# Performance work log

Hardware: AMD Instinct MI355X
Metric: run time of the kernel (lower is better)

## Reference

```python
import jax, jax.numpy as jnp
import numpy as np

CHUNK = 64
EMA_DECAY = 0.99


def setup_inputs() -> dict:
    key = jax.random.key(0)
    ks = jax.random.split(key, 4)
    Bsz, S, H, P, N = 2, 4096, 16, 64, 128
    X = jax.random.normal(ks[0], (Bsz, S, H, P), jnp.float32)
    # negative log-decay rates, as in Mamba-2 (A = -softplus(...) style)
    A = -jnp.abs(jax.random.normal(ks[1], (Bsz, S, H), jnp.float32)) * 0.1
    Bm = jax.random.normal(ks[2], (Bsz, S, H, N), jnp.float32) / np.sqrt(N)
    Cm = jax.random.normal(ks[3], (Bsz, S, H, N), jnp.float32) / np.sqrt(N)
    # ChunkedSurpriseGate parameters / buffers
    log2_alpha_base = jnp.full((H,), -0.15, jnp.float32)
    log2_beta = jnp.zeros((H,), jnp.float32)
    surprise_ema = jnp.ones((H,), jnp.float32)
    return {"X": X, "A": A, "Bm": Bm, "Cm": Cm,
            "log2_alpha_base": log2_alpha_base, "log2_beta": log2_beta,
            "surprise_ema": surprise_ema}


def _chunked_surprise_ssd(X, A, Bm, Cm, log2_alpha_base, log2_beta, surprise_ema):
    Bsz, S, H, P = X.shape
    N = Bm.shape[-1]
    cs = CHUNK
    nC = S // cs  # seqlen chosen divisible by chunk_size (no padding branch)

    # [B, nC, cs, H, ...] -> chunk-major [nC, B, H, cs, ...] for lax.scan
    Xc = X.reshape(Bsz, nC, cs, H, P).transpose(1, 0, 3, 2, 4)   # [nC,B,H,cs,P]
    Ac = A.reshape(Bsz, nC, cs, H).transpose(1, 0, 3, 2)          # [nC,B,H,cs]
    Bc = Bm.reshape(Bsz, nC, cs, H, N).transpose(1, 0, 3, 2, 4)   # [nC,B,H,cs,N]
    Cc = Cm.reshape(Bsz, nC, cs, H, N).transpose(1, 0, 3, 2, 4)   # [nC,B,H,cs,N]

    idx = jnp.arange(cs)
    tri = idx[:, None] >= idx[None, :]  # causal mask for decay matrix L

    # gate constants (per-head)
    alpha_base = 1.0 - jnp.exp2(jnp.clip(log2_alpha_base, -3.32, -0.015))  # [H]
    beta = jnp.exp2(jnp.clip(log2_beta, -2.0, 2.0))                         # [H]

    def step(carry, xs):
        h_prev, h_before, decay_prev, ema = carry
        c, X_c, A_c, B_c, C_c = xs
        first = c == 0

        # --- delayed state-based surprise: ||h_prev - decay_prev * h_before||^2
        err = jnp.mean((h_prev - decay_prev[..., None, None] * h_before) ** 2,
                       axis=(-2, -1))  # [B,H]
        # EMA update (training=True path; torch does it under no_grad)
        ema_new = jax.lax.stop_gradient(EMA_DECAY * ema + (1.0 - EMA_DECAY) * jnp.mean(err, axis=0))
        normalized = err / (ema_new[None, :] + 1e-6)                # [B,H]
        boost = jax.nn.relu(jnp.tanh(beta[None, :] * normalized))
        alpha = jnp.clip(alpha_base[None, :] + (1.0 - alpha_base[None, :]) * boost,
                         0.01, 0.999)
        # torch: decay_scale = (1-alpha).mean().item()  -> detached scalar
        ds = jax.lax.stop_gradient(jnp.mean(1.0 - alpha))
        decay_scale = jnp.where(first, jnp.float32(1.0), ds)
        ema_out = jnp.where(first, ema, ema_new)  # no gate call on chunk 0

        # --- single-chunk SSD ---
        Acs = jnp.cumsum(A_c * decay_scale, axis=-1)                 # [B,H,cs]
        # causal decay matrix L[i,j] = exp(Acs[i]-Acs[j]) for i>=j
        L = jnp.where(tri, jnp.exp(Acs[..., :, None] - Acs[..., None, :]), 0.0)
        CB = jnp.einsum('bhin,bhjn->bhij', C_c, B_c)
        Y_intra = jnp.einsum('bhij,bhjd->bhid', L * CB, X_c)
        decay_from_start = jnp.exp(Acs)                               # [B,H,cs]
        Y_inter = jnp.einsum('bhin,bhnd,bhi->bhid', C_c, h_prev, decay_from_start)
        decay_to_end = jnp.exp(Acs[..., -1:] - Acs)                   # [B,H,cs]
        h_contrib = jnp.einsum('bhtn,bhtd,bht->bhnd', B_c, X_c, decay_to_end)
        decay_total = jnp.exp(Acs[..., -1])                           # [B,H]
        h_end = decay_total[..., None, None] * h_prev + h_contrib

        return (h_end, h_prev, decay_total, ema_out), Y_intra + Y_inter

    h0 = jnp.zeros((Bsz, H, N, P), X.dtype)
    carry0 = (h0, h0, jnp.ones((Bsz, H), X.dtype), surprise_ema)
    xs = (jnp.arange(nC), Xc, Ac, Bc, Cc)
    _, Ys = jax.lax.scan(step, carry0, xs)  # [nC,B,H,cs,P]

    # stack dim=2, permute(0,2,3,1,4), reshape -> [B,S,H,P]
    Y = Ys.transpose(1, 0, 3, 2, 4).reshape(Bsz, S, H, P)
    return Y


def reference(X, A, Bm, Cm, log2_alpha_base, log2_beta, surprise_ema):
    return _chunked_surprise_ssd(X, A, Bm, Cm, log2_alpha_base, log2_beta, surprise_ema)
```

## Files before the change

### kernel.cpp

```cpp
#include <hip/hip_runtime.h>
#include <math.h>


#define CSZ 64
#define NCH 64
#define NHD 16
#define PD  64
#define ND  128
#define BHN 32
#define NTILES 2048
#define GGRID 64
#define SEQ 4096

#define WS_S   0
#define WS_EG  131072
#define WS_DS  262144
#define WS_HC  262400

using bf16x8 = __attribute__((ext_vector_type(8))) short;
using f32x4  = __attribute__((ext_vector_type(4))) float;

__device__ __forceinline__ short f2bf(float f) {
  union { float f; unsigned u; } v; v.f = f;
  unsigned r = (v.u + 0x7FFFu + ((v.u >> 16) & 1u)) >> 16;
  return (short)r;
}

__device__ __forceinline__ float bf2f(short s) {
  union { float f; unsigned u; } v;
  v.u = ((unsigned)(unsigned short)s) << 16;
  return v.f;
}

__device__ __forceinline__ void split4(float4 v, short4& hi, short4& lo) {
  hi.x = f2bf(v.x); lo.x = f2bf(v.x - bf2f(hi.x));
  hi.y = f2bf(v.y); lo.y = f2bf(v.y - bf2f(hi.y));
  hi.z = f2bf(v.z); lo.z = f2bf(v.z - bf2f(hi.z));
  hi.w = f2bf(v.w); lo.w = f2bf(v.w - bf2f(hi.w));
}

__global__ __launch_bounds__(256) void k_gramerr(
    const float* __restrict__ X, const float* __restrict__ A,
    const float* __restrict__ Bm, float* __restrict__ ws)
{
  __shared__ __align__(16) short BhiS[64*136];
  __shared__ __align__(16) short BloS[64*136];
  __shared__ __align__(16) short XhiS[64*72];
  __shared__ __align__(16) short XloS[64*72];
  __shared__ float Sl[CSZ];
  __shared__ float Zl[CSZ];
  short* Mhi = BhiS;
  short* Mlo = BloS;
  short* Uhi = XhiS;
  short* Ulo = XloS;

  const int tile = blockIdx.x;
  const int c  = tile & 63;
  const int bh = tile >> 6;
  const int b = bh >> 4, h = bh & 15;
  const int tid = threadIdx.x;

  if (tid < CSZ) {
    float v = A[(size_t)(b*SEQ + c*CSZ + tid)*NHD + h];
    #pragma unroll
    for (int d = 1; d < 64; d <<= 1) {
      float n = __shfl_up(v, d);
      if (tid >= d) v += n;
    }
    Sl[tid] = v;
    ws[WS_S + tile*CSZ + tid] = v;
  }

  {
    const float* Bbase = Bm + ((size_t)(b*SEQ + c*CSZ)*NHD + h)*ND;
    #pragma unroll
    for (int qq = 0; qq < 8; ++qq) {
      int lin = qq*256 + tid;
      int t = lin >> 5, n4 = (lin & 31)*4;
      float4 v = *(const float4*)(Bbase + (size_t)t*(NHD*ND) + n4);
      short4 hi, lo; split4(v, hi, lo);
      *(short4*)&BhiS[t*136 + n4] = hi;
      *(short4*)&BloS[t*136 + n4] = lo;
    }
    const float* Xbase = X + ((size_t)(b*SEQ + c*CSZ)*NHD + h)*PD;
    #pragma unroll
    for (int qq = 0; qq < 4; ++qq) {
      int lin = qq*256 + tid;
      int t = lin >> 4, p4 = (lin & 15)*4;
      float4 v = *(const float4*)(Xbase + (size_t)t*(NHD*PD) + p4);
      short4 hi, lo; split4(v, hi, lo);
      *(short4*)&XhiS[t*72 + p4] = hi;
      *(short4*)&XloS[t*72 + p4] = lo;
    }
  }
  __syncthreads();

  if (tid < CSZ) Zl[tid] = Sl[63] - Sl[tid];

  const int w = tid >> 6;
  const int lane = tid & 63;
  const int m = lane & 15, q = lane >> 4;

  f32x4 z4 = {0.f,0.f,0.f,0.f};
  f32x4 gb[4], gx[4];
  #pragma unroll
  for (int i = 0; i < 4; ++i) { gb[i] = z4; gx[i] = z4; }

  #pragma unroll
  for (int kk = 0; kk < 4; ++kk) {
    const int ao = (w*16+m)*136 + kk*32 + q*8;
    bf16x8 ah = *(bf16x8*)&BhiS[ao];
    bf16x8 al = *(bf16x8*)&BloS[ao];
    #pragma unroll
    for (int ct = 0; ct < 4; ++ct) {
      const int bo = (ct*16+m)*136 + kk*32 + q*8;
      bf16x8 bhv = *(bf16x8*)&BhiS[bo];
      bf16x8 blv = *(bf16x8*)&BloS[bo];
      gb[ct] = __builtin_amdgcn_mfma_f32_16x16x32_bf16(ah, bhv, gb[ct], 0,0,0);
      gb[ct] = __builtin_amdgcn_mfma_f32_16x16x32_bf16(ah, blv, gb[ct], 0,0,0);
      gb[ct] = __builtin_amdgcn_mfma_f32_16x16x32_bf16(al, bhv, gb[ct], 0,0,0);
    }
  }
  #pragma unroll
  for (int kk = 0; kk < 2; ++kk) {
    const int ao = (w*16+m)*72 + kk*32 + q*8;
    bf16x8 ah = *(bf16x8*)&XhiS[ao];
    bf16x8 al = *(bf16x8*)&XloS[ao];
    #pragma unroll
    for (int ct = 0; ct < 4; ++ct) {
      const int bo = (ct*16+m)*72 + kk*32 + q*8;
      bf16x8 bhv = *(bf16x8*)&XhiS[bo];
      bf16x8 blv = *(bf16x8*)&XloS[bo];
      gx[ct] = __builtin_amdgcn_mfma_f32_16x16x32_bf16(ah, bhv, gx[ct], 0,0,0);
      gx[ct] = __builtin_amdgcn_mfma_f32_16x16x32_bf16(ah, blv, gx[ct], 0,0,0);
      gx[ct] = __builtin_amdgcn_mfma_f32_16x16x32_bf16(al, bhv, gx[ct], 0,0,0);
    }
  }
  __syncthreads();

  #pragma unroll
  for (int ct = 0; ct < 4; ++ct)
    #pragma unroll
    for (int r = 0; r < 4; ++r) {
      int i = w*16 + q*4 + r;
      int j = ct*16 + m;
      float mvf = gb[ct][r]*gx[ct][r]*(1.0f/8192.0f);
      short mh = f2bf(mvf);
      Mhi[i*72 + j] = mh;
      Mlo[i*72 + j] = f2bf(mvf - bf2f(mh));
    }
  #pragma unroll
  for (int qq = 0; qq < 16; ++qq) {
    int idx = qq*256 + tid;
    int g = idx >> 6, t = idx & 63;
    float u = expf(((float)g*(1.0f/63.0f))*Zl[t]);
    short uh = f2bf(u);
    Uhi[g*72 + t] = uh;
    Ulo[g*72 + t] = f2bf(u - bf2f(uh));
  }
  __syncthreads();

  f32x4 wv4[4];
  #pragma unroll
  for (int i = 0; i < 4; ++i) wv4[i] = z4;
  #pragma unroll
  for (int kk = 0; kk < 2; ++kk) {
    const int ao = (w*16+m)*72 + kk*32 + q*8;
    bf16x8 uh = *(bf16x8*)&Uhi[ao];
    bf16x8 ul = *(bf16x8*)&Ulo[ao];
    #pragma unroll
    for (int ct = 0; ct < 4; ++ct) {
      const int bo = (ct*16+m)*72 + kk*32 + q*8;
      bf16x8 mh = *(bf16x8*)&Mhi[bo];
      bf16x8 ml = *(bf16x8*)&Mlo[bo];
      wv4[ct] = __builtin_amdgcn_mfma_f32_16x16x32_bf16(uh, mh, wv4[ct], 0,0,0);
      wv4[ct] = __builtin_amdgcn_mfma_f32_16x16x32_bf16(uh, ml, wv4[ct], 0,0,0);
      wv4[ct] = __builtin_amdgcn_mfma_f32_16x16x32_bf16(ul, mh, wv4[ct], 0,0,0);
    }
  }

  #pragma unroll
  for (int r = 0; r < 4; ++r) {
    int g = w*16 + q*4 + r;
    float e = 0.f;
    #pragma unroll
    for (int ct = 0; ct < 4; ++ct) {
      int t = ct*16 + m;
      float uval = bf2f(Uhi[g*72 + t]) + bf2f(Ulo[g*72 + t]);
      e += wv4[ct][r] * uval;
    }
    e += __shfl_xor(e, 1);
    e += __shfl_xor(e, 2);
    e += __shfl_xor(e, 4);
    e += __shfl_xor(e, 8);
    if (m == 0) ws[WS_EG + (c*GGRID + g)*BHN + bh] = e;
  }
}

__global__ __launch_bounds__(64) void k_gate(
    const float* __restrict__ l2ab, const float* __restrict__ l2b,
    const float* __restrict__ sema, float* __restrict__ ws)
{
  const int lane = threadIdx.x;
  const int h = lane & 15;
  float ab = 0.f, bt = 1.f, ema = 0.f;
  if (lane < NHD) {
    float la = fminf(fmaxf(l2ab[lane], -3.32f), -0.015f);
    ab = 1.0f - exp2f(la);
    float lb = fminf(fmaxf(l2b[lane], -2.0f), 2.0f);
    bt = exp2f(lb);
    ema = sema[lane];
  }
  const float ab_bh = __shfl(ab, h);
  const float bt_bh = __shfl(bt, h);
  float ds_prev = 1.0f;
  if (lane == 0) ws[WS_DS + 0] = 1.0f;
  const float* EG = ws + WS_EG;
  for (int c = 1; c < NCH; ++c) {
    const int j = c - 1;
    float x = ds_prev * 63.0f;
    int ib = (int)floorf(x);
    ib = max(1, min(61, ib));
    float u = x - (float)ib;
    float err = 0.f;
    if (lane < BHN) {
      const float* p = EG + ((size_t)j*GGRID + (ib-1))*BHN + lane;
      float ym1 = p[0], y0 = p[32], y1 = p[64], y2 = p[96];
      err = ym1*(u*(u-1.f)*(u-2.f))*(-1.f/6.f)
          + y0 *((u+1.f)*(u-1.f)*(u-2.f))*(0.5f)
          + y1 *((u+1.f)*u*(u-2.f))*(-0.5f)
          + y2 *((u+1.f)*u*(u-1.f))*(1.f/6.f);
    }
    float e0 = __shfl(err, h);
    float e1 = __shfl(err, 16 + h);
    float ema_new = 0.99f*ema + 0.01f*0.5f*(e0 + e1);
    float emv = __shfl(ema_new, h);
    float oma = 0.f;
    if (lane < BHN) {
      float normalized = err / (emv + 1e-6f);
      float boost = fmaxf(tanhf(bt_bh*normalized), 0.f);
      float alpha = ab_bh + (1.f - ab_bh)*boost;
      alpha = fminf(fmaxf(alpha, 0.01f), 0.999f);
      oma = 1.f - alpha;
    }
    float s = oma;
    s += __shfl_xor(s, 1);  s += __shfl_xor(s, 2);  s += __shfl_xor(s, 4);
    s += __shfl_xor(s, 8);  s += __shfl_xor(s, 16);
    float ds = __shfl(s, 0) * (1.0f/32.0f);
    if (lane < NHD) ema = ema_new;
    if (lane == 0) ws[WS_DS + c] = ds;
    ds_prev = ds;
  }
}

__global__ __launch_bounds__(256, 2) void k_chunk(
    const float* __restrict__ X, const float* __restrict__ Bm,
    const float* __restrict__ Cm, float* __restrict__ ws,
    float* __restrict__ Y)
{
  __shared__ short Cs[64*136];
  __shared__ short Bs[64*136];
  __shared__ short BsTw[128*72];
  __shared__ short XsT[64*72];
  __shared__ short Es[64*72];
  __shared__ float Acs[CSZ];
  __shared__ float Wl[CSZ];

  const int tile = blockIdx.x;
  const int c  = tile & 63;
  const int bh = tile >> 6;
  const int b = bh >> 4, h = bh & 15;
  const int tid = threadIdx.x;

  const float dsc = ws[WS_DS + c];
  if (tid < CSZ) {
    float sv  = ws[WS_S + tile*CSZ + tid];
    float s63 = ws[WS_S + tile*CSZ + 63];
    Acs[tid] = dsc*sv;
    Wl[tid]  = expf(dsc*(s63 - sv));
  }
  __syncthreads();

  const float* Bbase = Bm + ((size_t)(b*SEQ + c*CSZ)*NHD + h)*ND;
  const float* Cbase = Cm + ((size_t)(b*SEQ + c*CSZ)*NHD + h)*ND;
  const float* Xbase = X  + ((size_t)(b*SEQ + c*CSZ)*NHD + h)*PD;
  #pragma unroll
  for (int qq = 0; qq < 8; ++qq) {
    int lin = qq*256 + tid;
    int t = lin >> 5, n4 = (lin & 31)*4;
    float4 cv = *(const float4*)(Cbase + (size_t)t*(NHD*ND) + n4);
    short4 cs4; cs4.x=f2bf(cv.x); cs4.y=f2bf(cv.y); cs4.z=f2bf(cv.z); cs4.w=f2bf(cv.w);
    *(short4*)&Cs[t*136 + n4] = cs4;
    float4 bv = *(const float4*)(Bbase + (size_t)t*(NHD*ND) + n4);
    short4 bs4; bs4.x=f2bf(bv.x); bs4.y=f2bf(bv.y); bs4.z=f2bf(bv.z); bs4.w=f2bf(bv.w);
    *(short4*)&Bs[t*136 + n4] = bs4;
    float wt = Wl[t];
    BsTw[(n4+0)*72 + t] = f2bf(bv.x*wt);
    BsTw[(n4+1)*72 + t] = f2bf(bv.y*wt);
    BsTw[(n4+2)*72 + t] = f2bf(bv.z*wt);
    BsTw[(n4+3)*72 + t] = f2bf(bv.w*wt);
  }
  #pragma unroll
  for (int qq = 0; qq < 4; ++qq) {
    int lin = qq*256 + tid;
    int t = lin >> 4, p4 = (lin & 15)*4;
    float4 xv = *(const float4*)(Xbase + (size_t)t*(NHD*PD) + p4);
    XsT[(p4+0)*72 + t] = f2bf(xv.x);
    XsT[(p4+1)*72 + t] = f2bf(xv.y);
    XsT[(p4+2)*72 + t] = f2bf(xv.z);
    XsT[(p4+3)*72 + t] = f2bf(xv.w);
  }
  __syncthreads();

  const int w = tid >> 6;
  const int lane = tid & 63;
  const int m = lane & 15, q = lane >> 4;

  f32x4 acc0 = {0.f,0.f,0.f,0.f}, acc1 = acc0, acc2 = acc0, acc3 = acc0;
  #pragma unroll
  for (int kk = 0; kk < 4; ++kk) {
    bf16x8 af = *(bf16x8*)&Cs[(w*16+m)*136 + kk*32 + q*8];
    bf16x8 b0 = *(bf16x8*)&Bs[( 0+m)*136 + kk*32 + q*8];
    bf16x8 b1 = *(bf16x8*)&Bs[(16+m)*136 + kk*32 + q*8];
    bf16x8 b2 = *(bf16x8*)&Bs[(32+m)*136 + kk*32 + q*8];
    bf16x8 b3 = *(bf16x8*)&Bs[(48+m)*136 + kk*32 + q*8];
    acc0 = __builtin_amdgcn_mfma_f32_16x16x32_bf16(af, b0, acc0, 0,0,0);
    acc1 = __builtin_amdgcn_mfma_f32_16x16x32_bf16(af, b1, acc1, 0,0,0);
    acc2 = __builtin_amdgcn_mfma_f32_16x16x32_bf16(af, b2, acc2, 0,0,0);
    acc3 = __builtin_amdgcn_mfma_f32_16x16x32_bf16(af, b3, acc3, 0,0,0);
  }
  {
    f32x4 accs[4] = {acc0, acc1, acc2, acc3};
    #pragma unroll
    for (int ct = 0; ct < 4; ++ct) {
      int j = ct*16 + m;
      float aj = Acs[j];
      #pragma unroll
      for (int r = 0; r < 4; ++r) {
        int i = w*16 + q*4 + r;
        float v = (i >= j) ? expf(Acs[i]-aj)*accs[ct][r] : 0.f;
        Es[i*72 + j] = f2bf(v);
      }
    }
  }

  f32x4 h00={0.f,0.f,0.f,0.f}, h01=h00, h02=h00, h03=h00;
  f32x4 h10=h00, h11=h00, h12=h00, h13=h00;
  #pragma unroll
  for (int kk = 0; kk < 2; ++kk) {
    bf16x8 a0 = *(bf16x8*)&BsTw[((2*w+0)*16+m)*72 + kk*32 + q*8];
    bf16x8 a1 = *(bf16x8*)&BsTw[((2*w+1)*16+m)*72 + kk*32 + q*8];
    bf16x8 x0 = *(bf16x8*)&XsT[( 0+m)*72 + kk*32 + q*8];
    bf16x8 x1 = *(bf16x8*)&XsT[(16+m)*72 + kk*32 + q*8];
    bf16x8 x2 = *(bf16x8*)&XsT[(32+m)*72 + kk*32 + q*8];
    bf16x8 x3 = *(bf16x8*)&XsT[(48+m)*72 + kk*32 + q*8];
    h00 = __builtin_amdgcn_mfma_f32_16x16x32_bf16(a0, x0, h00, 0,0,0);
    h01 = __builtin_amdgcn_mfma_f32_16x16x32_bf16(a0, x1, h01, 0,0,0);
    h02 = __builtin_amdgcn_mfma_f32_16x16x32_bf16(a0, x2, h02, 0,0,0);
    h03 = __builtin_amdgcn_mfma_f32_16x16x32_bf16(a0, x3, h03, 0,0,0);
    h10 = __builtin_amdgcn_mfma_f32_16x16x32_bf16(a1, x0, h10, 0,0,0);
    h11 = __builtin_amdgcn_mfma_f32_16x16x32_bf16(a1, x1, h11, 0,0,0);
    h12 = __builtin_amdgcn_mfma_f32_16x16x32_bf16(a1, x2, h12, 0,0,0);
    h13 = __builtin_amdgcn_mfma_f32_16x16x32_bf16(a1, x3, h13, 0,0,0);
  }

  f32x4 y0={0.f,0.f,0.f,0.f}, y1=y0, y2=y0, y3=y0;
  #pragma unroll
  for (int kk = 0; kk < 2; ++kk) {
    bf16x8 ef = *(bf16x8*)&Es[(w*16+m)*72 + kk*32 + q*8];
    bf16x8 x0 = *(bf16x8*)&XsT[( 0+m)*72 + kk*32 + q*8];
    bf16x8 x1 = *(bf16x8*)&XsT[(16+m)*72 + kk*32 + q*8];
    bf16x8 x2 = *(bf16x8*)&XsT[(32+m)*72 + kk*32 + q*8];
    bf16x8 x3 = *(bf16x8*)&XsT[(48+m)*72 + kk*32 + q*8];
    y0 = __builtin_amdgcn_mfma_f32_16x16x32_bf16(ef, x0, y0, 0,0,0);
    y1 = __builtin_amdgcn_mfma_f32_16x16x32_bf16(ef, x1, y1, 0,0,0);
    y2 = __builtin_amdgcn_mfma_f32_16x16x32_bf16(ef, x2, y2, 0,0,0);
    y3 = __builtin_amdgcn_mfma_f32_16x16x32_bf16(ef, x3, y3, 0,0,0);
  }

  {
    float* Ybase = Y + ((size_t)(b*SEQ + c*CSZ)*NHD + h)*PD;
    f32x4 ys[4] = {y0, y1, y2, y3};
    #pragma unroll
    for (int r = 0; r < 4; ++r) {
      int i = w*16 + q*4 + r;
      #pragma unroll
      for (int ct = 0; ct < 4; ++ct)
        Ybase[(size_t)i*(NHD*PD) + ct*16 + m] = ys[ct][r];
    }
  }
  {
    float* hcp = ws + WS_HC + (size_t)tile*(ND*PD);
    f32x4 hs[2][4] = {{h00,h01,h02,h03},{h10,h11,h12,h13}};
    #pragma unroll
    for (int nt = 0; nt < 2; ++nt)
      #pragma unroll
      for (int r = 0; r < 4; ++r) {
        int n = (2*w+nt)*16 + q*4 + r;
        #pragma unroll
        for (int pt = 0; pt < 4; ++pt)
          hcp[n*PD + pt*16 + m] = hs[nt][pt][r];
      }
  }
}

__global__ __launch_bounds__(256) void k_scan(float* __restrict__ ws)
{
  __shared__ float dtbl[NCH];
  const int bh = blockIdx.x >> 3, part = blockIdx.x & 7;
  const int tid = threadIdx.x;
  if (tid < NCH) {
    float s63 = ws[WS_S + (bh*NCH + tid)*CSZ + 63];
    dtbl[tid] = expf(ws[WS_DS + tid]*s63);
  }
  __syncthreads();
  float* base = ws + WS_HC + (size_t)bh*(NCH*ND*PD) + part*1024 + tid*4;
  float4 h4 = make_float4(0.f, 0.f, 0.f, 0.f);
  #pragma unroll 1
  for (int c = 0; c < NCH; ++c) {
    float4* p = (float4*)(base + (size_t)c*(ND*PD));
    float4 v = *p;
    *p = h4;
    float dt = dtbl[c];
    h4.x = dt*h4.x + v.x;  h4.y = dt*h4.y + v.y;
    h4.z = dt*h4.z + v.z;  h4.w = dt*h4.w + v.w;
  }
}

__global__ __launch_bounds__(256, 4) void k_inter(
    const float* __restrict__ Cm, float* __restrict__ ws,
    float* __restrict__ Y)
{
  __shared__ short Cs[64*136];
  __shared__ short HsT[64*136];
  __shared__ float Dfs[CSZ];

  const int tile = blockIdx.x;
  const int c  = tile & 63;
  const int bh = tile >> 6;
  const int b = bh >> 4, h = bh & 15;
  const int tid = threadIdx.x;

  const float dsc = ws[WS_DS + c];
  if (tid < CSZ) Dfs[tid] = expf(dsc*ws[WS_S + tile*CSZ + tid]);

  const float* Cbase = Cm + ((size_t)(b*SEQ + c*CSZ)*NHD + h)*ND;
  const float* hp = ws + WS_HC + (size_t)tile*(ND*PD);
  #pragma unroll
  for (int qq = 0; qq < 8; ++qq) {
    int lin = qq*256 + tid;
    int t = lin >> 5, n4 = (lin & 31)*4;
    float4 cv = *(const float4*)(Cbase + (size_t)t*(NHD*ND) + n4);
    short4 cs4; cs4.x=f2bf(cv.x); cs4.y=f2bf(cv.y); cs4.z=f2bf(cv.z); cs4.w=f2bf(cv.w);
    *(short4*)&Cs[t*136 + n4] = cs4;
    int n = lin >> 4, p4 = (lin & 15)*4;
    float4 hv = *(const float4*)(hp + (size_t)lin*4);
    HsT[(p4+0)*136 + n] = f2bf(hv.x);
    HsT[(p4+1)*136 + n] = f2bf(hv.y);
    HsT[(p4+2)*136 + n] = f2bf(hv.z);
    HsT[(p4+3)*136 + n] = f2bf(hv.w);
  }
  __syncthreads();

  const int w = tid >> 6;
  const int lane = tid & 63;
  const int m = lane & 15, q = lane >> 4;

  f32x4 a0 = {0.f,0.f,0.f,0.f}, a1 = a0, a2 = a0, a3 = a0;
  #pragma unroll
  for (int kk = 0; kk < 4; ++kk) {
    bf16x8 cf = *(bf16x8*)&Cs[(w*16+m)*136 + kk*32 + q*8];
    bf16x8 hb0 = *(bf16x8*)&HsT[( 0+m)*136 + kk*32 + q*8];
    bf16x8 hb1 = *(bf16x8*)&HsT[(16+m)*136 + kk*32 + q*8];
    bf16x8 hb2 = *(bf16x8*)&HsT[(32+m)*136 + kk*32 + q*8];
    bf16x8 hb3 = *(bf16x8*)&HsT[(48+m)*136 + kk*32 + q*8];
    a0 = __builtin_amdgcn_mfma_f32_16x16x32_bf16(cf, hb0, a0, 0,0,0);
    a1 = __builtin_amdgcn_mfma_f32_16x16x32_bf16(cf, hb1, a1, 0,0,0);
    a2 = __builtin_amdgcn_mfma_f32_16x16x32_bf16(cf, hb2, a2, 0,0,0);
    a3 = __builtin_amdgcn_mfma_f32_16x16x32_bf16(cf, hb3, a3, 0,0,0);
  }

  float* Ybase = Y + ((size_t)(b*SEQ + c*CSZ)*NHD + h)*PD;
  f32x4 as[4] = {a0, a1, a2, a3};
  #pragma unroll
  for (int r = 0; r < 4; ++r) {
    int i = w*16 + q*4 + r;
    float d = Dfs[i];
    #pragma unroll
    for (int ct = 0; ct < 4; ++ct) {
      size_t idx = (size_t)i*(NHD*PD) + ct*16 + m;
      Ybase[idx] += d*as[ct][r];
    }
  }
}

extern "C" void kernel_launch(void* const* d_in, const int* in_sizes, int n_in,
                              void* d_out, int out_size, void* d_ws, size_t ws_size,
                              hipStream_t stream) {
  const float* X    = (const float*)d_in[0];
  const float* A    = (const float*)d_in[1];
  const float* Bm   = (const float*)d_in[2];
  const float* Cm   = (const float*)d_in[3];
  const float* l2ab = (const float*)d_in[4];
  const float* l2b  = (const float*)d_in[5];
  const float* sema = (const float*)d_in[6];
  float* Y  = (float*)d_out;
  float* ws = (float*)d_ws;

  hipLaunchKernelGGL(k_gramerr, dim3(NTILES), dim3(256), 0, stream, X, A, Bm, ws);
  hipLaunchKernelGGL(k_gate,    dim3(1),      dim3(64),  0, stream, l2ab, l2b, sema, ws);
  hipLaunchKernelGGL(k_chunk,   dim3(NTILES), dim3(256), 0, stream, X, Bm, Cm, ws, Y);
  hipLaunchKernelGGL(k_scan,    dim3(256),    dim3(256), 0, stream, ws);
  hipLaunchKernelGGL(k_inter,   dim3(NTILES), dim3(256), 0, stream, Cm, ws, Y);
}
```

Baseline: 344.8 us.

## Stage gate error grid in LDS, load C fragments directly, widen scan grid

In k_gate, the per-chunk error grid is double-buffered in shared memory with a register prefetch of the next chunk, so the serial loop no longer waits on dependent global loads. In k_chunk, the C operand is loaded straight from global memory into MFMA fragments in registers, and the Es buffer reuses the Bs buffer (with an added barrier). Dropping two LDS arrays lets launch bounds rise to 3 blocks per CU. k_scan runs on 4x more blocks with scalar instead of float4 elements, giving more parallelism to the latency-bound recurrence, at the cost of narrower memory accesses.

Result: slower. 367.4 us (+6.6%).

```diff
diff --git a/kernel.cpp b/kernel.cpp
--- a/kernel.cpp
+++ b/kernel.cpp
@@ -201,6 +201,7 @@
     const float* __restrict__ l2ab, const float* __restrict__ l2b,
     const float* __restrict__ sema, float* __restrict__ ws)
 {
+  __shared__ float EGs[2][GGRID*BHN];
   const int lane = threadIdx.x;
   const int h = lane & 15;
   float ab = 0.f, bt = 1.f, ema = 0.f;
@@ -213,18 +214,30 @@
   }
   const float ab_bh = __shfl(ab, h);
   const float bt_bh = __shfl(bt, h);
+  const float* EG = ws + WS_EG;
+  {
+    const float4* src = (const float4*)EG;
+    float4* dst = (float4*)EGs[0];
+    #pragma unroll
+    for (int r = 0; r < 8; ++r) dst[r*64 + lane] = src[r*64 + lane];
+  }
   float ds_prev = 1.0f;
   if (lane == 0) ws[WS_DS + 0] = 1.0f;
-  const float* EG = ws + WS_EG;
   for (int c = 1; c < NCH; ++c) {
-    const int j = c - 1;
+    const int cur = (c - 1) & 1;
+    float4 pf[8];
+    if (c < NCH-1) {
+      const float4* src = (const float4*)(EG + (size_t)c*(GGRID*BHN));
+      #pragma unroll
+      for (int r = 0; r < 8; ++r) pf[r] = src[r*64 + lane];
+    }
     float x = ds_prev * 63.0f;
     int ib = (int)floorf(x);
     ib = max(1, min(61, ib));
     float u = x - (float)ib;
     float err = 0.f;
     if (lane < BHN) {
-      const float* p = EG + ((size_t)j*GGRID + (ib-1))*BHN + lane;
+      const float* p = &EGs[cur][(ib-1)*BHN + lane];
       float ym1 = p[0], y0 = p[32], y1 = p[64], y2 = p[96];
       err = ym1*(u*(u-1.f)*(u-2.f))*(-1.f/6.f)
           + y0 *((u+1.f)*(u-1.f)*(u-2.f))*(0.5f)
@@ -250,27 +263,46 @@
     if (lane < NHD) ema = ema_new;
     if (lane == 0) ws[WS_DS + c] = ds;
     ds_prev = ds;
-  }
-}
-
-__global__ __launch_bounds__(256, 2) void k_chunk(
+    if (c < NCH-1) {
+      float4* dst = (float4*)EGs[c & 1];
+      #pragma unroll
+      for (int r = 0; r < 8; ++r) dst[r*64 + lane] = pf[r];
+    }
+  }
+}
+
+__global__ __launch_bounds__(256, 3) void k_chunk(
     const float* __restrict__ X, const float* __restrict__ Bm,
     const float* __restrict__ Cm, float* __restrict__ ws,
     float* __restrict__ Y)
 {
-  __shared__ short Cs[64*136];
   __shared__ short Bs[64*136];
   __shared__ short BsTw[128*72];
   __shared__ short XsT[64*72];
-  __shared__ short Es[64*72];
   __shared__ float Acs[CSZ];
   __shared__ float Wl[CSZ];
+  short* Es = Bs;
 
   const int tile = blockIdx.x;
   const int c  = tile & 63;
   const int bh = tile >> 6;
   const int b = bh >> 4, h = bh & 15;
   const int tid = threadIdx.x;
+  const int w = tid >> 6;
+  const int lane = tid & 63;
+  const int m = lane & 15, q = lane >> 4;
+
+  const float* Bbase = Bm + ((size_t)(b*SEQ + c*CSZ)*NHD + h)*ND;
+  const float* Cbase = Cm + ((size_t)(b*SEQ + c*CSZ)*NHD + h)*ND;
+  const float* Xbase = X  + ((size_t)(b*SEQ + c*CSZ)*NHD + h)*PD;
+
+  const float* crow = Cbase + (size_t)(w*16 + m)*(NHD*ND);
+  float4 cflo[4], cfhi[4];
+  #pragma unroll
+  for (int kk = 0; kk < 4; ++kk) {
+    cflo[kk] = *(const float4*)(crow + kk*32 + q*8);
+    cfhi[kk] = *(const float4*)(crow + kk*32 + q*8 + 4);
+  }
 
   const float dsc = ws[WS_DS + c];
   if (tid < CSZ) {
@@ -281,16 +313,10 @@
   }
   __syncthreads();
 
-  const float* Bbase = Bm + ((size_t)(b*SEQ + c*CSZ)*NHD + h)*ND;
-  const float* Cbase = Cm + ((size_t)(b*SEQ + c*CSZ)*NHD + h)*ND;
-  const float* Xbase = X  + ((size_t)(b*SEQ + c*CSZ)*NHD + h)*PD;
   #pragma unroll
   for (int qq = 0; qq < 8; ++qq) {
     int lin = qq*256 + tid;
     int t = lin >> 5, n4 = (lin & 31)*4;
-    float4 cv = *(const float4*)(Cbase + (size_t)t*(NHD*ND) + n4);
-    short4 cs4; cs4.x=f2bf(cv.x); cs4.y=f2bf(cv.y); cs4.z=f2bf(cv.z); cs4.w=f2bf(cv.w);
-    *(short4*)&Cs[t*136 + n4] = cs4;
     float4 bv = *(const float4*)(Bbase + (size_t)t*(NHD*ND) + n4);
     short4 bs4; bs4.x=f2bf(bv.x); bs4.y=f2bf(bv.y); bs4.z=f2bf(bv.z); bs4.w=f2bf(bv.w);
     *(short4*)&Bs[t*136 + n4] = bs4;
@@ -312,23 +338,29 @@
   }
   __syncthreads();
 
-  const int w = tid >> 6;
-  const int lane = tid & 63;
-  const int m = lane & 15, q = lane >> 4;
+  bf16x8 af[4];
+  #pragma unroll
+  for (int kk = 0; kk < 4; ++kk) {
+    bf16x8 t;
+    t[0]=f2bf(cflo[kk].x); t[1]=f2bf(cflo[kk].y); t[2]=f2bf(cflo[kk].z); t[3]=f2bf(cflo[kk].w);
+    t[4]=f2bf(cfhi[kk].x); t[5]=f2bf(cfhi[kk].y); t[6]=f2bf(cfhi[kk].z); t[7]=f2bf(cfhi[kk].w);
+    af[kk] = t;
+  }
 
   f32x4 acc0 = {0.f,0.f,0.f,0.f}, acc1 = acc0, acc2 = acc0, acc3 = acc0;
   #pragma unroll
   for (int kk = 0; kk < 4; ++kk) {
-    bf16x8 af = *(bf16x8*)&Cs[(w*16+m)*136 + kk*32 + q*8];
     bf16x8 b0 = *(bf16x8*)&Bs[( 0+m)*136 + kk*32 + q*8];
     bf16x8 b1 = *(bf16x8*)&Bs[(16+m)*136 + kk*32 + q*8];
     bf16x8 b2 = *(bf16x8*)&Bs[(32+m)*136 + kk*32 + q*8];
     bf16x8 b3 = *(bf16x8*)&Bs[(48+m)*136 + kk*32 + q*8];
-    acc0 = __builtin_amdgcn_mfma_f32_16x16x32_bf16(af, b0, acc0, 0,0,0);
-    acc1 = __builtin_amdgcn_mfma_f32_16x16x32_bf16(af, b1, acc1, 0,0,0);
-    acc2 = __builtin_amdgcn_mfma_f32_16x16x32_bf16(af, b2, acc2, 0,0,0);
-    acc3 = __builtin_amdgcn_mfma_f32_16x16x32_bf16(af, b3, acc3, 0,0,0);
-  }
+    acc0 = __builtin_amdgcn_mfma_f32_16x16x32_bf16(af[kk], b0, acc0, 0,0,0);
+    acc1 = __builtin_amdgcn_mfma_f32_16x16x32_bf16(af[kk], b1, acc1, 0,0,0);
+    acc2 = __builtin_amdgcn_mfma_f32_16x16x32_bf16(af[kk], b2, acc2, 0,0,0);
+    acc3 = __builtin_amdgcn_mfma_f32_16x16x32_bf16(af[kk], b3, acc3, 0,0,0);
+  }
+  __syncthreads();
+
   {
     f32x4 accs[4] = {acc0, acc1, acc2, acc3};
     #pragma unroll
@@ -407,23 +439,21 @@
 __global__ __launch_bounds__(256) void k_scan(float* __restrict__ ws)
 {
   __shared__ float dtbl[NCH];
-  const int bh = blockIdx.x >> 3, part = blockIdx.x & 7;
+  const int bh = blockIdx.x >> 5, part = blockIdx.x & 31;
   const int tid = threadIdx.x;
   if (tid < NCH) {
     float s63 = ws[WS_S + (bh*NCH + tid)*CSZ + 63];
     dtbl[tid] = expf(ws[WS_DS + tid]*s63);
   }
   __syncthreads();
-  float* base = ws + WS_HC + (size_t)bh*(NCH*ND*PD) + part*1024 + tid*4;
-  float4 h4 = make_float4(0.f, 0.f, 0.f, 0.f);
+  float* base = ws + WS_HC + (size_t)bh*(NCH*ND*PD) + part*256 + tid;
+  float hacc = 0.f;
   #pragma unroll 1
   for (int c = 0; c < NCH; ++c) {
-    float4* p = (float4*)(base + (size_t)c*(ND*PD));
-    float4 v = *p;
-    *p = h4;
-    float dt = dtbl[c];
-    h4.x = dt*h4.x + v.x;  h4.y = dt*h4.y + v.y;
-    h4.z = dt*h4.z + v.z;  h4.w = dt*h4.w + v.w;
+    float* p = base + (size_t)c*(ND*PD);
+    float v = *p;
+    *p = hacc;
+    hacc = dtbl[c]*hacc + v;
   }
 }
 
@@ -510,6 +540,6 @@
   hipLaunchKernelGGL(k_gramerr, dim3(NTILES), dim3(256), 0, stream, X, A, Bm, ws);
   hipLaunchKernelGGL(k_gate,    dim3(1),      dim3(64),  0, stream, l2ab, l2b, sema, ws);
   hipLaunchKernelGGL(k_chunk,   dim3(NTILES), dim3(256), 0, stream, X, Bm, Cm, ws, Y);
-  hipLaunchKernelGGL(k_scan,    dim3(256),    dim3(256), 0, stream, ws);
+  hipLaunchKernelGGL(k_scan,    dim3(1024),   dim3(256), 0, stream, ws);
   hipLaunchKernelGGL(k_inter,   dim3(NTILES), dim3(256), 0, stream, Cm, ws, Y);
 }
```
